# Kernel optimization log

Measured on AMD Instinct MI355X. Metric: run time of the kernel, lower is better.

The kernel has to match this reference:

```python
import jax, jax.numpy as jnp
import numpy as np

D = 2          # in_out_dim
HID = 64       # hidden_dim of hypernet
WIDTH = 64     # number of rank-1 blocks
COND = 4       # condition_dim
BATCH = 262144
BLOCK = WIDTH * D


def setup_inputs() -> dict:
    key = jax.random.key(0)
    ks = jax.random.split(key, 8)
    s = lambda k, shape, scale: (jax.random.normal(k, shape, jnp.float32) * scale)
    return {
        "t": jax.random.uniform(ks[0], (1,), jnp.float32),
        "z": jax.random.normal(ks[1], (BATCH, D), jnp.float32),
        "logp_z": jnp.zeros((BATCH, 1), jnp.float32),
        "condition": jax.random.normal(ks[2], (BATCH, COND), jnp.float32),
        # HyperNetwork params (torch Linear convention: weight [out, in])
        "hn_w1": s(ks[3], (HID, 1), 1.0), "hn_b1": jnp.zeros((HID,), jnp.float32),
        "hn_w2": s(ks[4], (HID, HID), 1.0 / np.sqrt(HID)), "hn_b2": jnp.zeros((HID,), jnp.float32),
        "hn_w3": s(ks[5], (3 * BLOCK + WIDTH, HID), 1.0 / np.sqrt(HID)), "hn_b3": jnp.zeros((3 * BLOCK + WIDTH,), jnp.float32),
        # TanhSigmoidMultiplyCondition params
        "cl_wz": s(ks[6], (2 * D, D), 1.0 / np.sqrt(D)), "cl_bz": jnp.zeros((2 * D,), jnp.float32),
        "cl_wc": s(ks[7], (2 * D, COND), 1.0 / np.sqrt(COND)), "cl_bc": jnp.zeros((2 * D,), jnp.float32),
    }


def reference(t, z, logp_z, condition, hn_w1, hn_b1, hn_w2, hn_b2, hn_w3, hn_b3,
              cl_wz, cl_bz, cl_wc, cl_bc):
    # --- TanhSigmoidMultiplyCondition: gated fusion of z and condition ---
    in_act = z @ cl_wz.T + cl_bz + condition @ cl_wc.T + cl_bc   # [B, 2D]
    zc = jnp.tanh(in_act[:, :D]) * jax.nn.sigmoid(in_act[:, D:])  # [B, D]

    # --- HyperNetwork: t -> per-block weights W, B, U ---
    p = jnp.tanh(t.reshape(1, 1) @ hn_w1.T + hn_b1)
    p = jnp.tanh(p @ hn_w2.T + hn_b2)
    p = (p @ hn_w3.T + hn_b3).reshape(-1)          # [3*BLOCK + WIDTH]
    W = p[:BLOCK].reshape(WIDTH, D, 1)
    U = p[BLOCK:2 * BLOCK].reshape(WIDTH, 1, D)
    G = p[2 * BLOCK:3 * BLOCK].reshape(WIDTH, 1, D)
    U = U * jax.nn.sigmoid(G)
    Bb = p[3 * BLOCK:].reshape(WIDTH, 1, 1)

    def f(zz):  # velocity field dz/dt as a function of the conditioned z
        h = jnp.tanh(jnp.einsum('bd,wdo->wbo', zz, W) + Bb)  # [WIDTH, B, 1]
        return jnp.einsum('wbo,wod->bd', h, U) / WIDTH        # mean over WIDTH -> [B, D]

    dz_dt = f(zc)

    # trace of Jacobian d(dz_dt)/d(zc) via forward-mode JVPs over the D basis vectors
    eye = jnp.eye(D, dtype=zc.dtype)
    tangents = jax.vmap(
        lambda e: jax.jvp(f, (zc,), (jnp.broadcast_to(e, zc.shape),))[1]
    )(eye)                                   # [D, B, D]
    trace = jnp.einsum('ibi->b', tangents)   # sum of diagonal entries
    dlogp_z_dt = -trace.reshape(-1, 1)       # [B, 1]

    return (dz_dt, dlogp_z_dt, condition)
```

## Files before the change

kernel.cpp:

```cpp
#include <hip/hip_runtime.h>
#include <math.h>

#define D 2
#define HID 64
#define WIDTH 64
#define CONDDIM 4
#define BATCH 262144
#define BLK 128

static __device__ __forceinline__ float fexp2(float x){ return __builtin_amdgcn_exp2f(x); }
static __device__ __forceinline__ float frcp(float x){ return __builtin_amdgcn_rcpf(x); }

__global__ __launch_bounds__(256) void fused_ode_kernel(
    const float* __restrict__ t,
    const float* __restrict__ hw1, const float* __restrict__ hb1,
    const float* __restrict__ hw2, const float* __restrict__ hb2,
    const float* __restrict__ hw3, const float* __restrict__ hb3,
    const float4* __restrict__ z4,
    const float4* __restrict__ c4,
    const float* __restrict__ cl_wz, const float* __restrict__ cl_bz,
    const float* __restrict__ cl_wc, const float* __restrict__ cl_bc,
    float* __restrict__ out)
{
    __shared__ float p1s[HID];
    __shared__ float p2s[HID];
    __shared__ float p3s[3*BLK + WIDTH];
    __shared__ __align__(16) float ps[520];

    const int tid = threadIdx.x;
    const int gid = blockIdx.x * 256 + tid;
    const float L2E = 1.4426950408889634f;
    const float C2  = 2.885390081777927f;

    float4 zz = z4[gid];
    float4 cA = c4[2*gid];
    float4 cB = c4[2*gid+1];

    float wz[8], wc[16], bb[4];
    #pragma unroll
    for (int j = 0; j < 8;  ++j) wz[j] = cl_wz[j];
    #pragma unroll
    for (int j = 0; j < 16; ++j) wc[j] = cl_wc[j];
    #pragma unroll
    for (int j = 0; j < 4;  ++j) bb[j] = cl_bz[j] + cl_bc[j];

    if (tid < HID) p1s[tid] = tanhf(t[0]*hw1[tid] + hb1[tid]);
    __syncthreads();

    if (tid < HID) {
        float a0=0.f, a1=0.f, a2=0.f, a3=0.f;
        const float4* row = (const float4*)(hw2 + tid*HID);
        #pragma unroll 4
        for (int k = 0; k < HID/4; ++k) {
            float4 r = row[k];
            a0 = fmaf(p1s[4*k+0], r.x, a0);
            a1 = fmaf(p1s[4*k+1], r.y, a1);
            a2 = fmaf(p1s[4*k+2], r.z, a2);
            a3 = fmaf(p1s[4*k+3], r.w, a3);
        }
        p2s[tid] = tanhf(hb2[tid] + ((a0+a1)+(a2+a3)));
    }
    __syncthreads();

    {
        int r = tid;
        {
            float a0=0.f, a1=0.f, a2=0.f, a3=0.f;
            const float4* row = (const float4*)(hw3 + r*HID);
            #pragma unroll 4
            for (int k = 0; k < HID/4; ++k) {
                float4 rv = row[k];
                a0 = fmaf(p2s[4*k+0], rv.x, a0);
                a1 = fmaf(p2s[4*k+1], rv.y, a1);
                a2 = fmaf(p2s[4*k+2], rv.z, a2);
                a3 = fmaf(p2s[4*k+3], rv.w, a3);
            }
            p3s[r] = hb3[r] + ((a0+a1)+(a2+a3));
        }
        if (tid < 192) {
            int r2 = 256 + tid;
            float a0=0.f, a1=0.f, a2=0.f, a3=0.f;
            const float4* row = (const float4*)(hw3 + r2*HID);
            #pragma unroll 4
            for (int k = 0; k < HID/4; ++k) {
                float4 rv = row[k];
                a0 = fmaf(p2s[4*k+0], rv.x, a0);
                a1 = fmaf(p2s[4*k+1], rv.y, a1);
                a2 = fmaf(p2s[4*k+2], rv.z, a2);
                a3 = fmaf(p2s[4*k+3], rv.w, a3);
            }
            p3s[r2] = hb3[r2] + ((a0+a1)+(a2+a3));
        }
    }
    __syncthreads();

    if (tid < WIDTH) {
        const int w = tid;
        float W0 = p3s[2*w],        W1 = p3s[2*w+1];
        float U0 = p3s[BLK+2*w],    U1 = p3s[BLK+2*w+1];
        float G0 = p3s[2*BLK+2*w],  G1 = p3s[2*BLK+2*w+1];
        float Bb = p3s[3*BLK+w];
        U0 *= frcp(1.0f + fexp2(-G0*L2E));
        U1 *= frcp(1.0f + fexp2(-G1*L2E));
        float Us0 = U0 * (1.0f/WIDTH);
        float Us1 = U1 * (1.0f/WIDTH);
        float WUs = W0*Us0 + W1*Us1;
        ps[8*w+0] = W0*C2;
        ps[8*w+1] = W1*C2;
        ps[8*w+2] = Bb*C2;
        ps[8*w+3] = WUs;
        ps[8*w+4] = Us0;
        ps[8*w+5] = Us1;
        ps[8*w+6] = 0.0f;
        ps[8*w+7] = 0.0f;
        float s = WUs;
        #pragma unroll
        for (int off = 32; off > 0; off >>= 1) s += __shfl_down(s, off);
        if (w == 0) ps[512] = s;
    }
    __syncthreads();

    float a[4], b[4];
    #pragma unroll
    for (int j = 0; j < 4; ++j) {
        float ta = fmaf(zz.x, wz[2*j], fmaf(zz.y, wz[2*j+1], bb[j]));
        ta = fmaf(cA.x, wc[4*j], ta); ta = fmaf(cA.y, wc[4*j+1], ta);
        ta = fmaf(cA.z, wc[4*j+2], ta); ta = fmaf(cA.w, wc[4*j+3], ta);
        a[j] = ta;
        float tb = fmaf(zz.z, wz[2*j], fmaf(zz.w, wz[2*j+1], bb[j]));
        tb = fmaf(cB.x, wc[4*j], tb); tb = fmaf(cB.y, wc[4*j+1], tb);
        tb = fmaf(cB.z, wc[4*j+2], tb); tb = fmaf(cB.w, wc[4*j+3], tb);
        b[j] = tb;
    }
    float zc0A = fmaf(-2.0f, frcp(1.0f + fexp2(a[0]*C2)), 1.0f) * frcp(1.0f + fexp2(-a[2]*L2E));
    float zc1A = fmaf(-2.0f, frcp(1.0f + fexp2(a[1]*C2)), 1.0f) * frcp(1.0f + fexp2(-a[3]*L2E));
    float zc0B = fmaf(-2.0f, frcp(1.0f + fexp2(b[0]*C2)), 1.0f) * frcp(1.0f + fexp2(-b[2]*L2E));
    float zc1B = fmaf(-2.0f, frcp(1.0f + fexp2(b[1]*C2)), 1.0f) * frcp(1.0f + fexp2(-b[3]*L2E));

    float4* oc = (float4*)(out + 3*(size_t)BATCH);
    oc[2*gid]   = cA;
    oc[2*gid+1] = cB;

    const float4* __restrict__ P = (const float4*)ps;
    float acc0A=0.f, acc1A=0.f, trA=0.f;
    float acc0B=0.f, acc1B=0.f, trB=0.f;
    #pragma unroll 8
    for (int w = 0; w < WIDTH; ++w) {
        float4 pa = P[2*w];
        float4 pb = P[2*w+1];
        float preA = fmaf(pa.x, zc0A, fmaf(pa.y, zc1A, pa.z));
        float preB = fmaf(pa.x, zc0B, fmaf(pa.y, zc1B, pa.z));
        float hA = fmaf(-2.0f, frcp(1.0f + fexp2(preA)), 1.0f);
        float hB = fmaf(-2.0f, frcp(1.0f + fexp2(preB)), 1.0f);
        acc0A = fmaf(hA, pb.x, acc0A);  acc1A = fmaf(hA, pb.y, acc1A);
        acc0B = fmaf(hB, pb.x, acc0B);  acc1B = fmaf(hB, pb.y, acc1B);
        trA = fmaf(hA*hA, pa.w, trA);
        trB = fmaf(hB*hB, pa.w, trB);
    }
    float sWU = ps[512];

    ((float4*)out)[gid] = make_float4(acc0A, acc1A, acc0B, acc1B);
    ((float2*)(out + 2*(size_t)BATCH))[gid] = make_float2(trA - sWU, trB - sWU);
}

extern "C" void kernel_launch(void* const* d_in, const int* in_sizes, int n_in,
                              void* d_out, int out_size, void* d_ws, size_t ws_size,
                              hipStream_t stream) {
    const float* t         = (const float*)d_in[0];
    const float* z         = (const float*)d_in[1];
    const float* condition = (const float*)d_in[3];
    const float* hn_w1 = (const float*)d_in[4];
    const float* hn_b1 = (const float*)d_in[5];
    const float* hn_w2 = (const float*)d_in[6];
    const float* hn_b2 = (const float*)d_in[7];
    const float* hn_w3 = (const float*)d_in[8];
    const float* hn_b3 = (const float*)d_in[9];
    const float* cl_wz = (const float*)d_in[10];
    const float* cl_bz = (const float*)d_in[11];
    const float* cl_wc = (const float*)d_in[12];
    const float* cl_bc = (const float*)d_in[13];

    const int nthreads = BATCH / 2;
    const int block = 256;
    const int grid = nthreads / block;
    fused_ode_kernel<<<grid, block, 0, stream>>>(
        t, hn_w1, hn_b1, hn_w2, hn_b2, hn_w3, hn_b3,
        (const float4*)z, (const float4*)condition,
        cl_wz, cl_bz, cl_wc, cl_bc, (float*)d_out);
}
```

Baseline: 20.84 us.

## Use packed-FP32 rational tanh approximation and strided two-element per-thread mapping

```diff
diff --git a/kernel.cpp b/kernel.cpp
--- a/kernel.cpp
+++ b/kernel.cpp
@@ -4,19 +4,30 @@
 #define D 2
 #define HID 64
 #define WIDTH 64
-#define CONDDIM 4
 #define BATCH 262144
 #define BLK 128
 
+typedef float v2f __attribute__((ext_vector_type(2)));
+
 static __device__ __forceinline__ float fexp2(float x){ return __builtin_amdgcn_exp2f(x); }
 static __device__ __forceinline__ float frcp(float x){ return __builtin_amdgcn_rcpf(x); }
+
+static __device__ __forceinline__ v2f tanh_pk(v2f x) {
+    v2f lo = {-4.f, -4.f}, hi = {4.f, 4.f};
+    v2f t = __builtin_elementwise_min(__builtin_elementwise_max(x, lo), hi);
+    v2f u = t * t;
+    v2f num = t * (945.f + u * (105.f + u));
+    v2f den = 945.f + u * (420.f + 15.f * u);
+    v2f r; r.x = frcp(den.x); r.y = frcp(den.y);
+    return num * r;
+}
 
 __global__ __launch_bounds__(256) void fused_ode_kernel(
     const float* __restrict__ t,
     const float* __restrict__ hw1, const float* __restrict__ hb1,
     const float* __restrict__ hw2, const float* __restrict__ hb2,
     const float* __restrict__ hw3, const float* __restrict__ hb3,
-    const float4* __restrict__ z4,
+    const float* __restrict__ z,
     const float4* __restrict__ c4,
     const float* __restrict__ cl_wz, const float* __restrict__ cl_bz,
     const float* __restrict__ cl_wc, const float* __restrict__ cl_bc,
@@ -25,24 +36,19 @@
     __shared__ float p1s[HID];
     __shared__ float p2s[HID];
     __shared__ float p3s[3*BLK + WIDTH];
-    __shared__ __align__(16) float ps[520];
+    __shared__ __align__(16) float4 psA[WIDTH];
+    __shared__ __align__(8)  float2 psB[WIDTH];
+    __shared__ float sSum;
 
     const int tid = threadIdx.x;
-    const int gid = blockIdx.x * 256 + tid;
+    const int e1 = blockIdx.x * 512 + tid;
+    const int e2 = e1 + 256;
     const float L2E = 1.4426950408889634f;
-    const float C2  = 2.885390081777927f;
 
-    float4 zz = z4[gid];
-    float4 cA = c4[2*gid];
-    float4 cB = c4[2*gid+1];
-
-    float wz[8], wc[16], bb[4];
-    #pragma unroll
-    for (int j = 0; j < 8;  ++j) wz[j] = cl_wz[j];
-    #pragma unroll
-    for (int j = 0; j < 16; ++j) wc[j] = cl_wc[j];
-    #pragma unroll
-    for (int j = 0; j < 4;  ++j) bb[j] = cl_bz[j] + cl_bc[j];
+    float2 zA = ((const float2*)z)[e1];
+    float2 zB = ((const float2*)z)[e2];
+    float4 cA = c4[e1];
+    float4 cB = c4[e2];
 
     if (tid < HID) p1s[tid] = tanhf(t[0]*hw1[tid] + hb1[tid]);
     __syncthreads();
@@ -63,10 +69,9 @@
     __syncthreads();
 
     {
-        int r = tid;
         {
             float a0=0.f, a1=0.f, a2=0.f, a3=0.f;
-            const float4* row = (const float4*)(hw3 + r*HID);
+            const float4* row = (const float4*)(hw3 + tid*HID);
             #pragma unroll 4
             for (int k = 0; k < HID/4; ++k) {
                 float4 rv = row[k];
@@ -75,7 +80,7 @@
                 a2 = fmaf(p2s[4*k+2], rv.z, a2);
                 a3 = fmaf(p2s[4*k+3], rv.w, a3);
             }
-            p3s[r] = hb3[r] + ((a0+a1)+(a2+a3));
+            p3s[tid] = hb3[tid] + ((a0+a1)+(a2+a3));
         }
         if (tid < 192) {
             int r2 = 256 + tid;
@@ -105,62 +110,63 @@
         float Us0 = U0 * (1.0f/WIDTH);
         float Us1 = U1 * (1.0f/WIDTH);
         float WUs = W0*Us0 + W1*Us1;
-        ps[8*w+0] = W0*C2;
-        ps[8*w+1] = W1*C2;
-        ps[8*w+2] = Bb*C2;
-        ps[8*w+3] = WUs;
-        ps[8*w+4] = Us0;
-        ps[8*w+5] = Us1;
-        ps[8*w+6] = 0.0f;
-        ps[8*w+7] = 0.0f;
+        psA[w] = make_float4(W0, W1, Bb, WUs);
+        psB[w] = make_float2(Us0, Us1);
         float s = WUs;
         #pragma unroll
         for (int off = 32; off > 0; off >>= 1) s += __shfl_down(s, off);
-        if (w == 0) ps[512] = s;
+        if (w == 0) sSum = s;
     }
     __syncthreads();
 
-    float a[4], b[4];
+    float wz[8], wc[16], bbv[4];
+    #pragma unroll
+    for (int j = 0; j < 8;  ++j) wz[j] = cl_wz[j];
+    #pragma unroll
+    for (int j = 0; j < 16; ++j) wc[j] = cl_wc[j];
+    #pragma unroll
+    for (int j = 0; j < 4;  ++j) bbv[j] = cl_bz[j] + cl_bc[j];
+
+    v2f zv0 = {zA.x, zB.x}, zv1 = {zA.y, zB.y};
+    v2f cv0 = {cA.x, cB.x}, cv1 = {cA.y, cB.y};
+    v2f cv2 = {cA.z, cB.z}, cv3 = {cA.w, cB.w};
+
+    v2f act[4];
     #pragma unroll
     for (int j = 0; j < 4; ++j) {
-        float ta = fmaf(zz.x, wz[2*j], fmaf(zz.y, wz[2*j+1], bb[j]));
-        ta = fmaf(cA.x, wc[4*j], ta); ta = fmaf(cA.y, wc[4*j+1], ta);
-        ta = fmaf(cA.z, wc[4*j+2], ta); ta = fmaf(cA.w, wc[4*j+3], ta);
-        a[j] = ta;
-        float tb = fmaf(zz.z, wz[2*j], fmaf(zz.w, wz[2*j+1], bb[j]));
-        tb = fmaf(cB.x, wc[4*j], tb); tb = fmaf(cB.y, wc[4*j+1], tb);
-        tb = fmaf(cB.z, wc[4*j+2], tb); tb = fmaf(cB.w, wc[4*j+3], tb);
-        b[j] = tb;
+        v2f a = zv0*wz[2*j] + zv1*wz[2*j+1] + bbv[j];
+        a = a + cv0*wc[4*j] + cv1*wc[4*j+1] + cv2*wc[4*j+2] + cv3*wc[4*j+3];
+        act[j] = a;
     }
-    float zc0A = fmaf(-2.0f, frcp(1.0f + fexp2(a[0]*C2)), 1.0f) * frcp(1.0f + fexp2(-a[2]*L2E));
-    float zc1A = fmaf(-2.0f, frcp(1.0f + fexp2(a[1]*C2)), 1.0f) * frcp(1.0f + fexp2(-a[3]*L2E));
-    float zc0B = fmaf(-2.0f, frcp(1.0f + fexp2(b[0]*C2)), 1.0f) * frcp(1.0f + fexp2(-b[2]*L2E));
-    float zc1B = fmaf(-2.0f, frcp(1.0f + fexp2(b[1]*C2)), 1.0f) * frcp(1.0f + fexp2(-b[3]*L2E));
+    v2f th0 = tanh_pk(act[0]);
+    v2f th1 = tanh_pk(act[1]);
+    v2f sg0 = 0.5f + 0.5f*tanh_pk(act[2]*0.5f);
+    v2f sg1 = 0.5f + 0.5f*tanh_pk(act[3]*0.5f);
+    v2f zc0 = th0 * sg0;
+    v2f zc1 = th1 * sg1;
 
     float4* oc = (float4*)(out + 3*(size_t)BATCH);
-    oc[2*gid]   = cA;
-    oc[2*gid+1] = cB;
+    oc[e1] = cA;
+    oc[e2] = cB;
 
-    const float4* __restrict__ P = (const float4*)ps;
-    float acc0A=0.f, acc1A=0.f, trA=0.f;
-    float acc0B=0.f, acc1B=0.f, trB=0.f;
+    v2f acc0 = {0.f,0.f}, acc1 = {0.f,0.f}, tr = {0.f,0.f};
     #pragma unroll 8
     for (int w = 0; w < WIDTH; ++w) {
-        float4 pa = P[2*w];
-        float4 pb = P[2*w+1];
-        float preA = fmaf(pa.x, zc0A, fmaf(pa.y, zc1A, pa.z));
-        float preB = fmaf(pa.x, zc0B, fmaf(pa.y, zc1B, pa.z));
-        float hA = fmaf(-2.0f, frcp(1.0f + fexp2(preA)), 1.0f);
-        float hB = fmaf(-2.0f, frcp(1.0f + fexp2(preB)), 1.0f);
-        acc0A = fmaf(hA, pb.x, acc0A);  acc1A = fmaf(hA, pb.y, acc1A);
-        acc0B = fmaf(hB, pb.x, acc0B);  acc1B = fmaf(hB, pb.y, acc1B);
-        trA = fmaf(hA*hA, pa.w, trA);
-        trB = fmaf(hB*hB, pa.w, trB);
+        float4 pa = psA[w];
+        float2 pb = psB[w];
+        v2f pre = zc0*pa.x + zc1*pa.y + pa.z;
+        v2f h = tanh_pk(pre);
+        acc0 += h * pb.x;
+        acc1 += h * pb.y;
+        tr   += (h*h) * pa.w;
     }
-    float sWU = ps[512];
+    float s = sSum;
 
-    ((float4*)out)[gid] = make_float4(acc0A, acc1A, acc0B, acc1B);
-    ((float2*)(out + 2*(size_t)BATCH))[gid] = make_float2(trA - sWU, trB - sWU);
+    ((float2*)out)[e1] = make_float2(acc0.x, acc1.x);
+    ((float2*)out)[e2] = make_float2(acc0.y, acc1.y);
+    float* dl = out + 2*(size_t)BATCH;
+    dl[e1] = tr.x - s;
+    dl[e2] = tr.y - s;
 }
 
 extern "C" void kernel_launch(void* const* d_in, const int* in_sizes, int n_in,
@@ -180,11 +186,10 @@
     const float* cl_wc = (const float*)d_in[12];
     const float* cl_bc = (const float*)d_in[13];
 
-    const int nthreads = BATCH / 2;
     const int block = 256;
-    const int grid = nthreads / block;
+    const int grid = BATCH / 512;
     fused_ode_kernel<<<grid, block, 0, stream>>>(
         t, hn_w1, hn_b1, hn_w2, hn_b2, hn_w3, hn_b3,
-        (const float4*)z, (const float4*)condition,
+        z, (const float4*)condition,
         cl_wz, cl_bz, cl_wc, cl_bc, (float*)d_out);
 }
```

Measured after the change: 21.58 us. +3.6%, slower.
